# Kernel tuning notes

Hardware: AMD Instinct MI355X
Metric: run time of the kernel (lower is better)

Reference implementation:

```python
import jax, jax.numpy as jnp
import numpy as np

N = 6000          # nodes
E = 192000        # edges (avg degree 32)
D = 512           # input_dim
H = 512           # hidden_dim
O = 40            # output_dim (classes)
K = 4096          # codebook_size
LAMB_EDGE = 1.0
LAMB_NODE = 1.0
COMMIT_W = 0.25
EPS = 1e-12


def _graph_conv(x, W, b, src, dst):
    """DGL GraphConv with norm='both' + ReLU activation.
    out = relu( D_in^{-1/2} A D_out^{-1/2} x W + b )"""
    ones = jnp.ones((E,), x.dtype)
    deg_out = jnp.clip(jax.ops.segment_sum(ones, src, num_segments=N), 1.0)
    deg_in = jnp.clip(jax.ops.segment_sum(ones, dst, num_segments=N), 1.0)
    xs = x * jax.lax.rsqrt(deg_out)[:, None]          # scale by src out-degree
    agg = jax.ops.segment_sum(xs[src], dst, num_segments=N)  # gather-scatter
    agg = agg * jax.lax.rsqrt(deg_in)[:, None]        # scale by dst in-degree
    return jax.nn.relu(agg @ W + b)


def _l2norm(x):
    return x * jax.lax.rsqrt(jnp.sum(x * x, axis=-1, keepdims=True) + EPS)


def setup_inputs() -> dict:
    key = jax.random.key(0)
    ks = jax.random.split(key, 13)
    s = lambda d: 1.0 / np.sqrt(d)
    return {
        "feats": jax.random.normal(ks[0], (N, D), jnp.float32),
        "W1": jax.random.normal(ks[1], (D, D), jnp.float32) * s(D),
        "b1": jnp.zeros((D,), jnp.float32),
        "W2": jax.random.normal(ks[2], (D, H), jnp.float32) * s(D),
        "b2": jnp.zeros((H,), jnp.float32),
        "Wd1": jax.random.normal(ks[3], (D, D), jnp.float32) * s(D),
        "bd1": jnp.zeros((D,), jnp.float32),
        "Wd2": jax.random.normal(ks[4], (D, D), jnp.float32) * s(D),
        "bd2": jnp.zeros((D,), jnp.float32),
        "Wl": jax.random.normal(ks[5], (H, O), jnp.float32) * s(H),
        "bl": jnp.zeros((O,), jnp.float32),
        "codebook": jax.random.normal(ks[6], (K, D), jnp.float32),
        "src": jax.random.randint(ks[7], (E,), 0, N, jnp.int32),
        "dst": jax.random.randint(ks[8], (E,), 0, N, jnp.int32),
    }


def reference(feats, W1, b1, W2, b2, Wd1, bd1, Wd2, bd2, Wl, bl, codebook, src, dst):
    # dense adjacency (as the torch module materializes via to_dense())
    adj = jnp.zeros((N, N), feats.dtype).at[dst, src].add(1.0)

    # GraphConv layer 1 (dropout is identity in eval)
    h = _graph_conv(feats, W1, b1, src, dst)           # [N, D]

    # cosine-sim VectorQuantize
    hn = _l2norm(h)
    en = _l2norm(codebook)                             # [K, D]
    dist = hn @ en.T                                   # [N, K] cosine sims
    ind = jnp.argmax(dist, axis=-1)                    # [N]
    q = en[ind]                                        # quantize with normed codebook
    commit_loss = COMMIT_W * jnp.mean((jax.lax.stop_gradient(q) - h) ** 2)
    quantized = h + jax.lax.stop_gradient(q - h)       # straight-through

    quantized_edge = quantized @ Wd1 + bd1             # decoder_1
    quantized_node = quantized @ Wd2 + bd2             # decoder_2

    feature_rec_loss = LAMB_NODE * jnp.mean((h - quantized_node) ** 2)

    adj_q = quantized_edge @ quantized_edge.T          # [N, N]
    adj_q = (adj_q - adj_q.min()) / (adj_q.max() - adj_q.min())
    edge_rec_loss = LAMB_EDGE * jnp.sqrt(jnp.mean((adj - adj_q) ** 2))

    # GraphConv layer 2 + output linear
    h2 = _graph_conv(quantized_edge, W2, b2, src, dst) # [N, H]
    out = h2 @ Wl + bl                                 # [N, O]

    loss = feature_rec_loss + edge_rec_loss + commit_loss
    return out, loss, dist
```

## Files before the change

### kernel.cpp

```cpp
#include <hip/hip_runtime.h>

typedef unsigned int u32;
typedef unsigned long long u64;

#define NN_ 6000
#define EE_ 192000
#define DD_ 512
#define KK_ 4096
#define OO_ 40
#define HSZ (1 << 19)
#define HMASK (HSZ - 1)
#define MT_A 376
#define NB_N 47
#define WPACKE (32 * 16 * 512)

typedef __bf16 bf16x8 __attribute__((ext_vector_type(8)));
typedef float f32x4 __attribute__((ext_vector_type(4)));

__device__ __forceinline__ u32 okey(float f) {
    u32 u = __float_as_uint(f);
    return (u & 0x80000000u) ? ~u : (u | 0x80000000u);
}
__device__ __forceinline__ float dkey(u32 u) {
    u32 b = (u & 0x80000000u) ? (u ^ 0x80000000u) : ~u;
    return __uint_as_float(b);
}
__device__ __forceinline__ u64 packKey(float v, int col) {
    return ((u64)okey(v) << 32) | (u32)(~(u32)col);
}
__device__ __forceinline__ unsigned short f2bf_rne(float f) {
    u32 x = __float_as_uint(f);
    u32 r = x + 0x7fffu + ((x >> 16) & 1u);
    return (unsigned short)(r >> 16);
}
__device__ __forceinline__ void gld_lds16(void* l, const void* g) {
    __builtin_amdgcn_global_load_lds(
        (const __attribute__((address_space(1))) unsigned int*)g,
        (__attribute__((address_space(3))) unsigned int*)l, 16, 0, 0);
}
#define LGKM0 do { asm volatile("s_waitcnt lgkmcnt(0)" ::: "memory"); __builtin_amdgcn_sched_barrier(0); } while (0)

__global__ void k_deg(const int* __restrict__ src, const int* __restrict__ dst,
                      int* __restrict__ degout, int* __restrict__ degin) {
    int e = blockIdx.x * 256 + threadIdx.x;
    if (e >= EE_) return;
    atomicAdd(&degout[src[e]], 1);
    atomicAdd(&degin[dst[e]], 1);
}

__global__ void k_rsqrtdeg(const int* __restrict__ degout, const int* __restrict__ degin,
                           float* __restrict__ rout, float* __restrict__ rin) {
    int i = blockIdx.x * 256 + threadIdx.x;
    if (i >= NN_) return;
    int doV = degout[i]; if (doV < 1) doV = 1;
    int diV = degin[i];  if (diV < 1) diV = 1;
    rout[i] = rsqrtf((float)doV);
    rin[i]  = rsqrtf((float)diV);
}

__global__ void k_scan(const int* __restrict__ cnt, int* __restrict__ offs, int n) {
    __shared__ int buf[1024];
    __shared__ int carry;
    if (threadIdx.x == 0) { carry = 0; offs[0] = 0; }
    __syncthreads();
    for (int base = 0; base < n; base += 1024) {
        int i = base + threadIdx.x;
        int v = (i < n) ? cnt[i] : 0;
        buf[threadIdx.x] = v;
        __syncthreads();
        for (int off = 1; off < 1024; off <<= 1) {
            int t = (threadIdx.x >= off) ? buf[threadIdx.x - off] : 0;
            __syncthreads();
            buf[threadIdx.x] += t;
            __syncthreads();
        }
        if (i < n) offs[i + 1] = carry + buf[threadIdx.x];
        __syncthreads();
        if (threadIdx.x == 0) carry += buf[1023];
        __syncthreads();
    }
}

__global__ void k_fill(const int* __restrict__ src, const int* __restrict__ dst,
                       const int* __restrict__ offs, int* __restrict__ cursor,
                       int* __restrict__ esrc) {
    int e = blockIdx.x * 256 + threadIdx.x;
    if (e >= EE_) return;
    int d = dst[e];
    int pos = offs[d] + atomicAdd(&cursor[d], 1);
    esrc[pos] = src[e];
}

__device__ __forceinline__ void split8(const float* vals, uint4& hw, uint4& lw) {
    u32 h[4], l[4];
    #pragma unroll
    for (int j = 0; j < 4; ++j) {
        unsigned short h0 = f2bf_rne(vals[2*j]),   h1 = f2bf_rne(vals[2*j+1]);
        float hf0 = __uint_as_float((u32)h0 << 16), hf1 = __uint_as_float((u32)h1 << 16);
        unsigned short l0 = f2bf_rne(vals[2*j] - hf0), l1 = f2bf_rne(vals[2*j+1] - hf1);
        h[j] = (u32)h0 | ((u32)h1 << 16);
        l[j] = (u32)l0 | ((u32)l1 << 16);
    }
    hw = make_uint4(h[0], h[1], h[2], h[3]);
    lw = make_uint4(l[0], l[1], l[2], l[3]);
}

template<int UNW>
__global__ __launch_bounds__(256) void k_aggs(
    const float* __restrict__ X, const int* __restrict__ esrc,
    const int* __restrict__ offs, const float* __restrict__ rout,
    const float* __restrict__ rin,
    unsigned short* __restrict__ dh, unsigned short* __restrict__ dl,
    float* __restrict__ gacc) {
    __shared__ float packbuf[4][128];
    __shared__ float mred[4];
    int b = blockIdx.x;
    int xcd = b & 7;
    int slice = xcd >> 1;
    int w = threadIdx.x >> 6, lane = threadIdx.x & 63;
    int wid = ((((b >> 3) << 1) | (xcd & 1)) << 2) + w;
    const float* Xc = X + slice * 128 + lane * 2;
    float mrAcc = 0.f;
    for (int node = wid; node < NN_; node += 1024) {
        int beg = offs[node], end = offs[node + 1];
        float a0 = 0.f, a1 = 0.f, u0 = 0.f, u1 = 0.f;
        for (int e = beg; e < end; ) {
            int cnt = end - e; if (cnt > 64) cnt = 64;
            int sreg = 0; float wreg = 0.f;
            if (lane < cnt) { sreg = esrc[e + lane]; wreg = rout[sreg]; }
            int j = 0;
            for (; j + 4 <= cnt; j += 4) {
                int s0 = __shfl(sreg, j),     s1 = __shfl(sreg, j + 1);
                int s2 = __shfl(sreg, j + 2), s3 = __shfl(sreg, j + 3);
                float w0 = __shfl(wreg, j),     w1 = __shfl(wreg, j + 1);
                float w2 = __shfl(wreg, j + 2), w3 = __shfl(wreg, j + 3);
                float2 v0 = *(const float2*)(Xc + (size_t)s0 * DD_);
                float2 v1 = *(const float2*)(Xc + (size_t)s1 * DD_);
                float2 v2 = *(const float2*)(Xc + (size_t)s2 * DD_);
                float2 v3 = *(const float2*)(Xc + (size_t)s3 * DD_);
                a0 = fmaf(w0, v0.x, a0); a1 = fmaf(w0, v0.y, a1);
                a0 = fmaf(w1, v1.x, a0); a1 = fmaf(w1, v1.y, a1);
                a0 = fmaf(w2, v2.x, a0); a1 = fmaf(w2, v2.y, a1);
                a0 = fmaf(w3, v3.x, a0); a1 = fmaf(w3, v3.y, a1);
                if (UNW) {
                    u0 += (v0.x + v1.x) + (v2.x + v3.x);
                    u1 += (v0.y + v1.y) + (v2.y + v3.y);
                }
            }
            for (; j < cnt; ++j) {
                int sj = __shfl(sreg, j); float wj = __shfl(wreg, j);
                float2 v = *(const float2*)(Xc + (size_t)sj * DD_);
                a0 = fmaf(wj, v.x, a0); a1 = fmaf(wj, v.y, a1);
                if (UNW) { u0 += v.x; u1 += v.y; }
            }
            e += cnt;
        }
        float ri = rin[node];
        packbuf[w][lane * 2] = a0 * ri;
        packbuf[w][lane * 2 + 1] = a1 * ri;
        LGKM0;
        if (lane < 16) {
            uint4 hw, lw;
            split8(&packbuf[w][(lane >> 2) * 32 + (lane & 3) * 8], hw, lw);
            int kb = slice * 4 + (lane >> 2);
            int lo = (lane & 3) * 16 + (node & 15);
            size_t base = (((size_t)(node >> 4) * 16 + kb) * 64 + lo) * 8;
            *(uint4*)(dh + base) = hw;
            *(uint4*)(dl + base) = lw;
        }
        if (UNW) {
            float2 q = *(const float2*)(Xc + (size_t)node * DD_);
            mrAcc = fmaf(q.x, u0, mrAcc);
            mrAcc = fmaf(q.y, u1, mrAcc);
        }
    }
    if (UNW) {
        for (int off = 32; off; off >>= 1) mrAcc += __shfl_xor(mrAcc, off);
        if (lane == 0) mred[w] = mrAcc;
        __syncthreads();
        if (threadIdx.x == 0)
            atomicAdd(&gacc[5], mred[0] + mred[1] + mred[2] + mred[3]);
    }
}

__global__ __launch_bounds__(256) void k_cbscale(const float* __restrict__ cb,
                                                 float* __restrict__ scale, int nrows) {
    int w = threadIdx.x >> 6, lane = threadIdx.x & 63;
    for (int row = blockIdx.x * 4 + w; row < nrows; row += gridDim.x * 4) {
        const float4* p = (const float4*)(cb + (size_t)row * DD_);
        float4 x = p[lane], y = p[lane + 64];
        float s = x.x * x.x + x.y * x.y + x.z * x.z + x.w * x.w
                + y.x * y.x + y.y * y.y + y.z * y.z + y.w * y.w;
        for (int off = 32; off; off >>= 1) s += __shfl_xor(s, off);
        if (lane == 0) scale[row] = 1.0f / sqrtf(s + 1e-12f);
    }
}

__global__ __launch_bounds__(256) void k_pack(
    const float* __restrict__ src, const float* __restrict__ rowscale,
    const int* __restrict__ gidx, int nrows,
    unsigned short* __restrict__ dh, unsigned short* __restrict__ dl) {
    int u = threadIdx.x >> 6, lane = threadIdx.x & 63;
    int nmt = (nrows + 15) >> 4;
    for (int unit = blockIdx.x; unit < nmt * 4; unit += gridDim.x) {
        int mt = unit >> 2, kb = (unit & 3) * 4 + u;
        int gr = mt * 16 + (lane & 15);
        int k = kb * 32 + (lane >> 4) * 8;
        float vals[8] = {0.f,0.f,0.f,0.f,0.f,0.f,0.f,0.f};
        if (gr < nrows) {
            int row = gidx ? gidx[gr] : gr;
            float sc = rowscale ? rowscale[row] : 1.0f;
            const float4* p = (const float4*)(src + (size_t)row * DD_ + k);
            float4 a = p[0], bv = p[1];
            vals[0]=a.x*sc; vals[1]=a.y*sc; vals[2]=a.z*sc; vals[3]=a.w*sc;
            vals[4]=bv.x*sc; vals[5]=bv.y*sc; vals[6]=bv.z*sc; vals[7]=bv.w*sc;
        }
        uint4 hw, lw;
        split8(vals, hw, lw);
        size_t base = (((size_t)mt * 16 + kb) * 64 + lane) * 8;
        *(uint4*)(dh + base) = hw;
        *(uint4*)(dl + base) = lw;
    }
}

__global__ __launch_bounds__(256) void k_wpack(
    const float* __restrict__ W,
    unsigned short* __restrict__ dh, unsigned short* __restrict__ dl) {
    int u = threadIdx.x >> 6, lane = threadIdx.x & 63;
    int mt = blockIdx.x, kb = blockIdx.y * 4 + u;
    int n = mt * 16 + (lane & 15);
    int k = kb * 32 + (lane >> 4) * 8;
    float vals[8];
    #pragma unroll
    for (int j = 0; j < 8; ++j) vals[j] = W[(size_t)(k + j) * DD_ + n];
    uint4 hw, lw;
    split8(vals, hw, lw);
    size_t base = (((size_t)mt * 16 + kb) * 64 + lane) * 8;
    *(uint4*)(dh + base) = hw;
    *(uint4*)(dl + base) = lw;
}

template<int MODE, int THREE>
__global__ __launch_bounds__(256) void gemm_mfma(
    const unsigned short* __restrict__ Ah, const unsigned short* __restrict__ Al,
    const unsigned short* __restrict__ Bh, const unsigned short* __restrict__ Bl,
    float* __restrict__ Cout, const float* __restrict__ bias,
    const float* __restrict__ Ref, int relu, int Mrows,
    float* __restrict__ gacc, u32* __restrict__ minKey, u32* __restrict__ maxKey,
    const float* __restrict__ bias2) {
    int bx, by;
    if (MODE == 1) {
        int t = blockIdx.x;
        int bi = (int)((sqrtf(8.f * (float)t + 1.f) - 1.f) * 0.5f);
        while ((bi + 1) * (bi + 2) / 2 <= t) ++bi;
        while (bi * (bi + 1) / 2 > t) --bi;
        bx = bi; by = t - bi * (bi + 1) / 2;
    } else { bx = blockIdx.x; by = blockIdx.y; }
    int side = (MODE == 4) ? (bx >> 2) : 0;
    int bxe  = (MODE == 4) ? (bx & 3) : bx;
    __shared__ char lds[32768];
    __shared__ float wred0[4], wred1[4], wred2[4], wred3[4];
    int tid = threadIdx.x;
    int wave = tid >> 6, lane = tid & 63;
    int gmtA = by * 8, gmtB = bxe * 8;
    const unsigned short* garr; int gmt0;
    if (wave == 0)      { garr = Ah; gmt0 = gmtA; }
    else if (wave == 1) { garr = Al; gmt0 = gmtA; }
    else if (wave == 2) { garr = Bh + (size_t)side * 2 * WPACKE; gmt0 = gmtB; }
    else                { garr = Bl + (size_t)side * 2 * WPACKE; gmt0 = gmtB; }
    char* ldst = lds + wave * 8192;
    f32x4 acc[4][4];
    #pragma unroll
    for (int i = 0; i < 4; ++i)
        #pragma unroll
        for (int j = 0; j < 4; ++j) acc[i][j] = (f32x4){0.f, 0.f, 0.f, 0.f};
    float commitAcc = 0.f;
    int wm = wave >> 1, wn = wave & 1;
    for (int kb = 0; kb < 16; ++kb) {
        if (THREE || wave != 1) {
            #pragma unroll
            for (int t = 0; t < 8; ++t) {
                const char* g = (const char*)garr + (((size_t)(gmt0 + t) * 16 + kb) * 1024) + lane * 16;
                gld_lds16(ldst + t * 1024 + lane * 16, g);
            }
        }
        __syncthreads();
        if (MODE == 4 && bx == 4) {
            int rg = tid >> 1, half = tid & 1;
            int m = by * 128 + rg;
            if (m < Mrows) {
                int tt = rg >> 4, r = rg & 15;
                const float* hp = Ref + (size_t)m * DD_ + kb * 32 + half * 16;
                float4 h0 = ((const float4*)hp)[0], h1 = ((const float4*)hp)[1];
                float4 h2 = ((const float4*)hp)[2], h3 = ((const float4*)hp)[3];
                float hv[16] = {h0.x,h0.y,h0.z,h0.w, h1.x,h1.y,h1.z,h1.w,
                                h2.x,h2.y,h2.z,h2.w, h3.x,h3.y,h3.z,h3.w};
                #pragma unroll
                for (int j2 = 0; j2 < 16; ++j2) {
                    int sub = half * 2 + (j2 >> 3), j = j2 & 7;
                    int off = tt * 1024 + (sub * 16 + r) * 16 + j * 2;
                    u32 hb = *(const unsigned short*)(lds + off);
                    u32 lb = *(const unsigned short*)(lds + 8192 + off);
                    float q = __uint_as_float(hb << 16) + __uint_as_float(lb << 16);
                    float d = q - hv[j2];
                    commitAcc = fmaf(d, d, commitAcc);
                }
            }
        }
        bf16x8 a_h[4], a_l[4], b_h[4], b_l[4];
        #pragma unroll
        for (int i = 0; i < 4; ++i) {
            int at = wm * 4 + i, bt = wn * 4 + i;
            a_h[i] = *(const bf16x8*)(lds + 0     + at * 1024 + lane * 16);
            if (THREE) a_l[i] = *(const bf16x8*)(lds + 8192 + at * 1024 + lane * 16);
            b_h[i] = *(const bf16x8*)(lds + 16384 + bt * 1024 + lane * 16);
            b_l[i] = *(const bf16x8*)(lds + 24576 + bt * 1024 + lane * 16);
        }
        #pragma unroll
        for (int i = 0; i < 4; ++i)
            #pragma unroll
            for (int j = 0; j < 4; ++j) {
                acc[i][j] = __builtin_amdgcn_mfma_f32_16x16x32_bf16(a_h[i], b_h[j], acc[i][j], 0, 0, 0);
                acc[i][j] = __builtin_amdgcn_mfma_f32_16x16x32_bf16(a_h[i], b_l[j], acc[i][j], 0, 0, 0);
                if (THREE)
                    acc[i][j] = __builtin_amdgcn_mfma_f32_16x16x32_bf16(a_l[i], b_h[j], acc[i][j], 0, 0, 0);
            }
        __syncthreads();
    }
    int m_base = by * 128 + wm * 64;
    int n_base = bxe * 128 + wn * 64;
    int rq = lane >> 4, cc = lane & 15;
    if (MODE == 0) {
        #pragma unroll
        for (int i = 0; i < 4; ++i) {
            int m = m_base + i * 16 + rq * 4;
            #pragma unroll
            for (int j = 0; j < 4; ++j) {
                int n = n_base + j * 16 + cc;
                #pragma unroll
                for (int r = 0; r < 4; ++r) {
                    if (m + r < NN_) Cout[(size_t)(m + r) * KK_ + n] = acc[i][j][r];
                }
            }
        }
    } else if (MODE == 2 || (MODE == 4 && side == 0)) {
        #pragma unroll
        for (int i = 0; i < 4; ++i) {
            int m = m_base + i * 16 + rq * 4;
            #pragma unroll
            for (int j = 0; j < 4; ++j) {
                int n = n_base + j * 16 + cc;
                float bv = bias[n];
                #pragma unroll
                for (int r = 0; r < 4; ++r) {
                    if (m + r < Mrows) {
                        float v = acc[i][j][r] + bv;
                        if (relu) v = fmaxf(v, 0.f);
                        Cout[(size_t)(m + r) * DD_ + n] = v;
                    }
                }
            }
        }
    } else if (MODE == 3 || (MODE == 4 && side == 1)) {
        const float* bs = (MODE == 4) ? bias2 : bias;
        float s = 0.f;
        #pragma unroll
        for (int i = 0; i < 4; ++i) {
            int m = m_base + i * 16 + rq * 4;
            #pragma unroll
            for (int j = 0; j < 4; ++j) {
                int n = n_base + j * 16 + cc;
                float bv = bs[n];
                #pragma unroll
                for (int r = 0; r < 4; ++r) {
                    if (m + r < Mrows) {
                        float d = Ref[(size_t)(m + r) * DD_ + n] - (acc[i][j][r] + bv);
                        s = fmaf(d, d, s);
                    }
                }
            }
        }
        for (int off = 32; off; off >>= 1) s += __shfl_xor(s, off);
        if (lane == 0) wred0[wave] = s;
        if (MODE == 4 && bx == 4) {
            float c = commitAcc;
            for (int off = 32; off; off >>= 1) c += __shfl_xor(c, off);
            if (lane == 0) wred1[wave] = c;
        }
        __syncthreads();
        if (tid == 0) {
            atomicAdd(&gacc[3], wred0[0] + wred0[1] + wred0[2] + wred0[3]);
            if (MODE == 4 && bx == 4)
                atomicAdd(&gacc[2], wred1[0] + wred1[1] + wred1[2] + wred1[3]);
        }
    } else {
        float tsum = 0.f, tsq = 0.f, tmin = 3.4e38f, tmax = -3.4e38f;
        #pragma unroll
        for (int i = 0; i < 4; ++i) {
            #pragma unroll
            for (int j = 0; j < 4; ++j) {
                #pragma unroll
                for (int r = 0; r < 4; ++r) {
                    int m = m_base + i * 16 + rq * 4 + r;
                    int n = n_base + j * 16 + cc;
                    if (m < NN_ && n < NN_ && n >= m) {
                        float v = acc[i][j][r];
                        float w = (n > m) ? 2.f : 1.f;
                        tsum += w * v;
                        tsq  += w * v * v;
                        tmin = fminf(tmin, v);
                        tmax = fmaxf(tmax, v);
                    }
                }
            }
        }
        for (int off = 32; off; off >>= 1) {
            tsum += __shfl_xor(tsum, off);
            tsq  += __shfl_xor(tsq, off);
            tmin = fminf(tmin, __shfl_xor(tmin, off));
            tmax = fmaxf(tmax, __shfl_xor(tmax, off));
        }
        if (lane == 0) { wred0[wave] = tsum; wred1[wave] = tsq; wred2[wave] = tmin; wred3[wave] = tmax; }
        __syncthreads();
        if (tid == 0) {
            atomicAdd(&gacc[0], wred0[0] + wred0[1] + wred0[2] + wred0[3]);
            atomicAdd(&gacc[1], wred1[0] + wred1[1] + wred1[2] + wred1[3]);
            atomicMin(minKey, okey(fminf(fminf(wred2[0], wred2[1]), fminf(wred2[2], wred2[3]))));
            atomicMax(maxKey, okey(fmaxf(fmaxf(wred3[0], wred3[1]), fmaxf(wred3[2], wred3[3]))));
        }
    }
}

__global__ __launch_bounds__(256) void k_rescore(
    const float* __restrict__ dist, const float* __restrict__ h,
    const float* __restrict__ rnorm, const float* __restrict__ cb,
    const float* __restrict__ scale, int* __restrict__ ind) {
    int w = threadIdx.x >> 6, lane = threadIdx.x & 63;
    for (int row = blockIdx.x * 4 + w; row < NN_; row += gridDim.x * 4) {
        const float4* dr4 = (const float4*)(dist + (size_t)row * KK_);
        float4 vbuf[16];
        float lmax = -3.4e38f;
        #pragma unroll
        for (int it = 0; it < 16; ++it) {
            float4 v = dr4[lane + it * 64];
            vbuf[it] = v;
            lmax = fmaxf(lmax, fmaxf(fmaxf(v.x, v.y), fmaxf(v.z, v.w)));
        }
        for (int off = 32; off; off >>= 1) lmax = fmaxf(lmax, __shfl_xor(lmax, off));
        float thr = lmax - 1e-3f;
        float hr = rnorm[row];
        const float* hp = h + (size_t)row * DD_;
        u64 best = 0;
        #pragma unroll 1
        for (int it = 0; it < 16; ++it) {
            float4 v = vbuf[it];
            u32 m4 = (v.x >= thr ? 1u : 0u) | (v.y >= thr ? 2u : 0u)
                   | (v.z >= thr ? 4u : 0u) | (v.w >= thr ? 8u : 0u);
            u64 bal = __ballot(m4 != 0);
            while (bal) {
                int l = __ffsll((unsigned long long)bal) - 1;
                bal &= bal - 1;
                u32 mm = __shfl(m4, l);
                while (mm) {
                    int j = __ffs(mm) - 1;
                    mm &= mm - 1;
                    int col = (l + it * 64) * 4 + j;
                    const float* cp = cb + (size_t)col * DD_;
                    float dot = 0.f;
                    #pragma unroll
                    for (int jj = 0; jj < 8; ++jj)
                        dot = fmaf(hp[lane + jj * 64], cp[lane + jj * 64], dot);
                    for (int off = 32; off; off >>= 1) dot += __shfl_xor(dot, off);
                    u64 key = packKey(dot * hr * scale[col], col);
                    if (key > best) best = key;
                }
            }
        }
        if (lane == 0) ind[row] = (int)(~(u32)(best & 0xFFFFFFFFull));
    }
}

__global__ __launch_bounds__(256) void gemm_nn(
    const float* __restrict__ A, const float* __restrict__ B,
    const float* __restrict__ bias, float* __restrict__ C,
    int M, int Ncols, int Kdim) {
    __shared__ float As[16][68];
    __shared__ float Bs[16][68];
    int tid = threadIdx.x;
    int tx = tid & 15, ty = tid >> 4;
    int m0 = blockIdx.y * 64, n0 = blockIdx.x * 64;
    float cv[4][4] = {};
    int ar = tid >> 2;
    int ak = (tid & 3) << 2;
    int am = m0 + ar;
    const float* Arow = (am < M) ? (A + (size_t)am * Kdim) : nullptr;
    int bk = tid >> 4;
    int bn = (tid & 15) << 2;
    for (int k0 = 0; k0 < Kdim; k0 += 16) {
        float4 av = make_float4(0.f, 0.f, 0.f, 0.f);
        if (Arow) av = *(const float4*)(Arow + k0 + ak);
        As[ak + 0][ar] = av.x; As[ak + 1][ar] = av.y;
        As[ak + 2][ar] = av.z; As[ak + 3][ar] = av.w;
        float4 bv = make_float4(0.f, 0.f, 0.f, 0.f);
        if (n0 + bn < Ncols)
            bv = *(const float4*)(B + (size_t)(k0 + bk) * Ncols + n0 + bn);
        Bs[bk][bn + 0] = bv.x; Bs[bk][bn + 1] = bv.y;
        Bs[bk][bn + 2] = bv.z; Bs[bk][bn + 3] = bv.w;
        __syncthreads();
        #pragma unroll
        for (int kk = 0; kk < 16; ++kk) {
            float4 a4 = *(const float4*)&As[kk][ty << 2];
            float4 b4 = *(const float4*)&Bs[kk][tx << 2];
            float ax[4] = {a4.x, a4.y, a4.z, a4.w};
            float bx[4] = {b4.x, b4.y, b4.z, b4.w};
            #pragma unroll
            for (int i = 0; i < 4; ++i)
                #pragma unroll
                for (int j = 0; j < 4; ++j)
                    cv[i][j] = fmaf(ax[i], bx[j], cv[i][j]);
        }
        __syncthreads();
    }
    #pragma unroll
    for (int i = 0; i < 4; ++i) {
        int m = m0 + (ty << 2) + i;
        if (m >= M) continue;
        #pragma unroll
        for (int j = 0; j < 4; ++j) {
            int n = n0 + (tx << 2) + j;
            if (n >= Ncols) continue;
            C[(size_t)m * Ncols + n] = cv[i][j] + bias[n];
        }
    }
}

__global__ void k_hash(const int* __restrict__ src, const int* __restrict__ dst,
                       int* __restrict__ hkey, int* __restrict__ hcnt) {
    int e = blockIdx.x * 256 + threadIdx.x;
    if (e >= EE_) return;
    int key = dst[e] * NN_ + src[e];
    u32 h = ((u32)key * 2654435761u) & HMASK;
    while (true) {
        int old = atomicCAS(&hkey[h], -1, key);
        if (old == -1 || old == key) { atomicAdd(&hcnt[h], 1); break; }
        h = (h + 1) & HMASK;
    }
}

__global__ __launch_bounds__(256) void k_m2scan(const int* __restrict__ hcnt, float* __restrict__ gacc) {
    float s = 0.f;
    for (int i = blockIdx.x * 256 + threadIdx.x; i < HSZ; i += gridDim.x * 256) {
        float c = (float)hcnt[i];
        s = fmaf(c, c, s);
    }
    for (int off = 32; off; off >>= 1) s += __shfl_xor(s, off);
    __shared__ float w1[4];
    int lane = threadIdx.x & 63, wv = threadIdx.x >> 6;
    if (lane == 0) w1[wv] = s;
    __syncthreads();
    if (threadIdx.x == 0) atomicAdd(&gacc[4], w1[0] + w1[1] + w1[2] + w1[3]);
}

__global__ void k_final(const float* __restrict__ gacc, const u32* __restrict__ minKey,
                        const u32* __restrict__ maxKey, float* __restrict__ lossOut) {
    if (threadIdx.x != 0 || blockIdx.x != 0) return;
    double Rsum = gacc[0], Rsq = gacc[1], commitS = gacc[2], recS = gacc[3];
    double m2 = gacc[4], mr = gacc[5], ms = (double)EE_;
    double mn = (double)dkey(*minKey);
    double mx = (double)dkey(*maxKey);
    double den = mx - mn;
    double NN2 = (double)NN_ * (double)NN_;
    double sum_aq2 = (Rsq - 2.0 * mn * Rsum + NN2 * mn * mn) / (den * den);
    double sum_maq = (mr - mn * ms) / den;
    double total = sum_aq2 + m2 - 2.0 * sum_maq;
    double edge = sqrt(total / NN2);
    double commit = 0.25 * commitS / ((double)NN_ * (double)DD_);
    double rec = recS / ((double)NN_ * (double)DD_);
    *lossOut = (float)(rec + edge + commit);
}

extern "C" void kernel_launch(void* const* d_in, const int* in_sizes, int n_in,
                              void* d_out, int out_size, void* d_ws, size_t ws_size,
                              hipStream_t stream) {
    const float* feats = (const float*)d_in[0];
    const float* W1 = (const float*)d_in[1];
    const float* b1 = (const float*)d_in[2];
    const float* W2 = (const float*)d_in[3];
    const float* b2v = (const float*)d_in[4];
    const float* Wd1 = (const float*)d_in[5];
    const float* bd1 = (const float*)d_in[6];
    const float* Wd2 = (const float*)d_in[7];
    const float* bd2 = (const float*)d_in[8];
    const float* Wl = (const float*)d_in[9];
    const float* bl = (const float*)d_in[10];
    const float* cb = (const float*)d_in[11];
    const int* src = (const int*)d_in[12];
    const int* dst = (const int*)d_in[13];

    float* outF = (float*)d_out;
    float* lossOut = outF + (size_t)NN_ * OO_;
    float* distOut = lossOut + 1;

    char* w = (char*)d_ws;
    size_t off = 0;
    auto alloc = [&](size_t bytes) -> void* {
        void* p = w + off;
        off = (off + bytes + 255) & ~(size_t)255;
        return p;
    };
    float* gacc = (float*)alloc(64);
    u32* maxKey = (u32*)alloc(4);
    int* degin = (int*)alloc((size_t)NN_ * 4);
    int* degout = (int*)alloc((size_t)NN_ * 4);
    int* cursor = (int*)alloc((size_t)NN_ * 4);
    int* hcnt = (int*)alloc((size_t)HSZ * 4);
    size_t z0end = off;
    int* hkey = (int*)alloc((size_t)HSZ * 4);
    u32* minKey = (u32*)alloc(4);
    size_t z1end = off;
    int* offs = (int*)alloc((size_t)(NN_ + 1) * 4);
    int* esrc = (int*)alloc((size_t)EE_ * 4);
    float* rin = (float*)alloc((size_t)NN_ * 4);
    float* rout = (float*)alloc((size_t)NN_ * 4);
    int* ind = (int*)alloc((size_t)NN_ * 4);
    float* scale = (float*)alloc((size_t)KK_ * 4);
    float* rnorm = (float*)alloc((size_t)NN_ * 4);
    float* h = (float*)alloc((size_t)NN_ * DD_ * 4);
    float* QE = (float*)alloc((size_t)NN_ * DD_ * 4);
    const size_t NPACK = (size_t)MT_A * 16 * DD_;
    unsigned short* P1 = (unsigned short*)alloc(NPACK * 2 * 2);
    unsigned short* P2 = (unsigned short*)alloc(NPACK * 2 * 2);
    unsigned short* enp = (unsigned short*)alloc((size_t)KK_ * DD_ * 2 * 2);
    const size_t WPACK = (size_t)32 * 16 * DD_;
    unsigned short* W1p = (unsigned short*)alloc(WPACK * 2 * 2);
    unsigned short* Wd1p = (unsigned short*)alloc(WPACK * 2 * 2);
    unsigned short* Wd2p = (unsigned short*)alloc(WPACK * 2 * 2);
    unsigned short* W2p = (unsigned short*)alloc(WPACK * 2 * 2);

    unsigned short* aggp_h = P1,  *aggp_l = P1 + NPACK;
    unsigned short* qcp_h  = P1,  *qcp_l  = P1 + NPACK;
    unsigned short* ag2p_h = P1,  *ag2p_l = P1 + NPACK;
    unsigned short* hnp_h  = P2,  *hnp_l  = P2 + NPACK;
    unsigned short* QEp_h  = P2,  *QEp_l  = P2 + NPACK;
    unsigned short* enp_h  = enp, *enp_l  = enp + (size_t)KK_ * DD_;

    hipMemsetAsync(w, 0, z0end, stream);
    hipMemsetAsync(w + z0end, 0xFF, z1end - z0end, stream);

    const int TB = 256;
    k_deg<<<(EE_ + TB - 1) / TB, TB, 0, stream>>>(src, dst, degout, degin);
    k_rsqrtdeg<<<(NN_ + TB - 1) / TB, TB, 0, stream>>>(degout, degin, rout, rin);
    k_scan<<<1, 1024, 0, stream>>>(degin, offs, NN_);
    k_fill<<<(EE_ + TB - 1) / TB, TB, 0, stream>>>(src, dst, offs, cursor, esrc);
    k_wpack<<<dim3(32, 4), TB, 0, stream>>>(W1, W1p, W1p + WPACK);
    k_wpack<<<dim3(32, 4), TB, 0, stream>>>(Wd1, Wd1p, Wd1p + WPACK);
    k_wpack<<<dim3(32, 4), TB, 0, stream>>>(Wd2, Wd2p, Wd2p + WPACK);
    k_wpack<<<dim3(32, 4), TB, 0, stream>>>(W2, W2p, W2p + WPACK);
    k_aggs<0><<<1024, TB, 0, stream>>>(feats, esrc, offs, rout, rin, aggp_h, aggp_l, nullptr);
    gemm_mfma<2,1><<<dim3(4, NB_N), TB, 0, stream>>>(aggp_h, aggp_l, W1p, W1p + WPACK,
                                                     h, b1, nullptr, 1, NN_, nullptr, nullptr, nullptr, nullptr);
    k_cbscale<<<256, TB, 0, stream>>>(h, rnorm, NN_);
    k_cbscale<<<256, TB, 0, stream>>>(cb, scale, KK_);
    k_pack<<<512, TB, 0, stream>>>(h, rnorm, nullptr, NN_, hnp_h, hnp_l);
    k_pack<<<512, TB, 0, stream>>>(cb, scale, nullptr, KK_, enp_h, enp_l);
    gemm_mfma<0,0><<<dim3(KK_ / 128, NB_N), TB, 0, stream>>>(hnp_h, hnp_l, enp_h, enp_l,
                                                             distOut, nullptr, nullptr, 0, NN_,
                                                             nullptr, nullptr, nullptr, nullptr);
    k_rescore<<<1024, TB, 0, stream>>>(distOut, h, rnorm, cb, scale, ind);
    k_pack<<<512, TB, 0, stream>>>(cb, scale, ind, NN_, qcp_h, qcp_l);
    gemm_mfma<4,1><<<dim3(8, NB_N), TB, 0, stream>>>(qcp_h, qcp_l, Wd1p, Wd1p + WPACK,
                                                     QE, bd1, h, 0, NN_, gacc, nullptr, nullptr, bd2);
    k_pack<<<512, TB, 0, stream>>>(QE, nullptr, nullptr, NN_, QEp_h, QEp_l);
    gemm_mfma<1,1><<<NB_N * (NB_N + 1) / 2, TB, 0, stream>>>(QEp_h, QEp_l, QEp_h, QEp_l,
                                                             nullptr, nullptr, nullptr, 0, NN_,
                                                             gacc, minKey, maxKey, nullptr);
    k_hash<<<(EE_ + TB - 1) / TB, TB, 0, stream>>>(src, dst, hkey, hcnt);
    k_m2scan<<<512, TB, 0, stream>>>(hcnt, gacc);
    k_aggs<1><<<1024, TB, 0, stream>>>(QE, esrc, offs, rout, rin, ag2p_h, ag2p_l, gacc);
    gemm_mfma<2,1><<<dim3(4, NB_N), TB, 0, stream>>>(ag2p_h, ag2p_l, W2p, W2p + WPACK,
                                                     h, b2v, nullptr, 1, NN_, nullptr, nullptr, nullptr, nullptr);
    gemm_nn<<<dim3(1, 94), TB, 0, stream>>>(h, Wl, bl, outF, NN_, OO_, DD_);
    k_final<<<1, 64, 0, stream>>>(gacc, minKey, maxKey, lossOut);
}
```

Before: 681.0 us.

## Add dedicated 256x128-tile Gram kernel, fuse row-norm into pack, serial-chunk scan

A new gemm_rpass kernel replaces the triangular 128x128 MODE 1 path for the QE·QEᵀ min/max/sum reduction. Each block computes a 256x128 tile with eight accumulator rows per wave, and blocks are remapped over the upper triangle to cut redundant A/B loads and block count. The separate row-norm and pack kernels are merged into one row-oriented k_rowpack that computes the L2 scale and writes the packed bf16 hi/lo layout in one pass. k_scan now does a single-pass scan with 6 elements per thread instead of looping over 1024-element chunks. Risks are higher register pressure from acc[8][4] in the new kernel and uncoalesced scattered writes from the row-oriented pack.

```diff
diff --git a/kernel.cpp b/kernel.cpp
--- a/kernel.cpp
+++ b/kernel.cpp
@@ -59,25 +59,27 @@
 }
 
 __global__ void k_scan(const int* __restrict__ cnt, int* __restrict__ offs, int n) {
-    __shared__ int buf[1024];
-    __shared__ int carry;
-    if (threadIdx.x == 0) { carry = 0; offs[0] = 0; }
+    __shared__ int part[1024];
+    int t = threadIdx.x;
+    int base = t * 6;
+    int v[6]; int s = 0;
+    #pragma unroll
+    for (int j = 0; j < 6; ++j) { int i = base + j; v[j] = (i < n) ? cnt[i] : 0; s += v[j]; }
+    part[t] = s;
     __syncthreads();
-    for (int base = 0; base < n; base += 1024) {
-        int i = base + threadIdx.x;
-        int v = (i < n) ? cnt[i] : 0;
-        buf[threadIdx.x] = v;
-        __syncthreads();
-        for (int off = 1; off < 1024; off <<= 1) {
-            int t = (threadIdx.x >= off) ? buf[threadIdx.x - off] : 0;
-            __syncthreads();
-            buf[threadIdx.x] += t;
-            __syncthreads();
-        }
-        if (i < n) offs[i + 1] = carry + buf[threadIdx.x];
-        __syncthreads();
-        if (threadIdx.x == 0) carry += buf[1023];
-        __syncthreads();
+    for (int off = 1; off < 1024; off <<= 1) {
+        int x = (t >= off) ? part[t - off] : 0;
+        __syncthreads();
+        part[t] += x;
+        __syncthreads();
+    }
+    int run = (t > 0) ? part[t - 1] : 0;
+    if (t == 0) offs[0] = 0;
+    #pragma unroll
+    for (int j = 0; j < 6; ++j) {
+        int i = base + j;
+        run += v[j];
+        if (i < n) offs[i + 1] = run;
     }
 }
 
@@ -183,41 +185,30 @@
     }
 }
 
-__global__ __launch_bounds__(256) void k_cbscale(const float* __restrict__ cb,
-                                                 float* __restrict__ scale, int nrows) {
+template<int NORM>
+__global__ __launch_bounds__(256) void k_rowpack(
+    const float* __restrict__ src, const int* __restrict__ gidx,
+    const float* __restrict__ scaleIn, float* __restrict__ scaleOut, int nrows,
+    unsigned short* __restrict__ dh, unsigned short* __restrict__ dl) {
     int w = threadIdx.x >> 6, lane = threadIdx.x & 63;
-    for (int row = blockIdx.x * 4 + w; row < nrows; row += gridDim.x * 4) {
-        const float4* p = (const float4*)(cb + (size_t)row * DD_);
-        float4 x = p[lane], y = p[lane + 64];
-        float s = x.x * x.x + x.y * x.y + x.z * x.z + x.w * x.w
-                + y.x * y.x + y.y * y.y + y.z * y.z + y.w * y.w;
-        for (int off = 32; off; off >>= 1) s += __shfl_xor(s, off);
-        if (lane == 0) scale[row] = 1.0f / sqrtf(s + 1e-12f);
-    }
-}
-
-__global__ __launch_bounds__(256) void k_pack(
-    const float* __restrict__ src, const float* __restrict__ rowscale,
-    const int* __restrict__ gidx, int nrows,
-    unsigned short* __restrict__ dh, unsigned short* __restrict__ dl) {
-    int u = threadIdx.x >> 6, lane = threadIdx.x & 63;
-    int nmt = (nrows + 15) >> 4;
-    for (int unit = blockIdx.x; unit < nmt * 4; unit += gridDim.x) {
-        int mt = unit >> 2, kb = (unit & 3) * 4 + u;
-        int gr = mt * 16 + (lane & 15);
-        int k = kb * 32 + (lane >> 4) * 8;
-        float vals[8] = {0.f,0.f,0.f,0.f,0.f,0.f,0.f,0.f};
-        if (gr < nrows) {
-            int row = gidx ? gidx[gr] : gr;
-            float sc = rowscale ? rowscale[row] : 1.0f;
-            const float4* p = (const float4*)(src + (size_t)row * DD_ + k);
-            float4 a = p[0], bv = p[1];
-            vals[0]=a.x*sc; vals[1]=a.y*sc; vals[2]=a.z*sc; vals[3]=a.w*sc;
-            vals[4]=bv.x*sc; vals[5]=bv.y*sc; vals[6]=bv.z*sc; vals[7]=bv.w*sc;
-        }
+    for (int r = blockIdx.x * 4 + w; r < nrows; r += gridDim.x * 4) {
+        int rs = gidx ? gidx[r] : r;
+        const float4* p = (const float4*)(src + (size_t)rs * DD_);
+        float4 x = p[lane * 2], y = p[lane * 2 + 1];
+        float sc;
+        if (NORM) {
+            float s = x.x * x.x + x.y * x.y + x.z * x.z + x.w * x.w
+                    + y.x * y.x + y.y * y.y + y.z * y.z + y.w * y.w;
+            for (int off = 32; off; off >>= 1) s += __shfl_xor(s, off);
+            sc = 1.0f / sqrtf(s + 1e-12f);
+            if (scaleOut && lane == 0) scaleOut[r] = sc;
+        } else {
+            sc = scaleIn ? scaleIn[rs] : 1.0f;
+        }
+        float vals[8] = {x.x*sc, x.y*sc, x.z*sc, x.w*sc, y.x*sc, y.y*sc, y.z*sc, y.w*sc};
         uint4 hw, lw;
         split8(vals, hw, lw);
-        size_t base = (((size_t)mt * 16 + kb) * 64 + lane) * 8;
+        size_t base = (((size_t)(r >> 4) * 16 + (lane >> 2)) * 64 + (lane & 3) * 16 + (r & 15)) * 8;
         *(uint4*)(dh + base) = hw;
         *(uint4*)(dl + base) = lw;
     }
@@ -246,20 +237,12 @@
     const unsigned short* __restrict__ Bh, const unsigned short* __restrict__ Bl,
     float* __restrict__ Cout, const float* __restrict__ bias,
     const float* __restrict__ Ref, int relu, int Mrows,
-    float* __restrict__ gacc, u32* __restrict__ minKey, u32* __restrict__ maxKey,
-    const float* __restrict__ bias2) {
-    int bx, by;
-    if (MODE == 1) {
-        int t = blockIdx.x;
-        int bi = (int)((sqrtf(8.f * (float)t + 1.f) - 1.f) * 0.5f);
-        while ((bi + 1) * (bi + 2) / 2 <= t) ++bi;
-        while (bi * (bi + 1) / 2 > t) --bi;
-        bx = bi; by = t - bi * (bi + 1) / 2;
-    } else { bx = blockIdx.x; by = blockIdx.y; }
+    float* __restrict__ gacc, const float* __restrict__ bias2) {
+    int bx = blockIdx.x, by = blockIdx.y;
     int side = (MODE == 4) ? (bx >> 2) : 0;
     int bxe  = (MODE == 4) ? (bx & 3) : bx;
     __shared__ char lds[32768];
-    __shared__ float wred0[4], wred1[4], wred2[4], wred3[4];
+    __shared__ float wred0[4], wred1[4];
     int tid = threadIdx.x;
     int wave = tid >> 6, lane = tid & 63;
     int gmtA = by * 8, gmtB = bxe * 8;
@@ -361,8 +344,8 @@
                 }
             }
         }
-    } else if (MODE == 3 || (MODE == 4 && side == 1)) {
-        const float* bs = (MODE == 4) ? bias2 : bias;
+    } else {
+        const float* bs = bias2;
         float s = 0.f;
         #pragma unroll
         for (int i = 0; i < 4; ++i) {
@@ -393,41 +376,105 @@
             if (MODE == 4 && bx == 4)
                 atomicAdd(&gacc[2], wred1[0] + wred1[1] + wred1[2] + wred1[3]);
         }
-    } else {
-        float tsum = 0.f, tsq = 0.f, tmin = 3.4e38f, tmax = -3.4e38f;
-        #pragma unroll
-        for (int i = 0; i < 4; ++i) {
-            #pragma unroll
-            for (int j = 0; j < 4; ++j) {
+    }
+}
+
+__global__ __launch_bounds__(256) void gemm_rpass(
+    const unsigned short* __restrict__ Qh, const unsigned short* __restrict__ Ql,
+    float* __restrict__ gacc, u32* __restrict__ minKey, u32* __restrict__ maxKey) {
+    int Lp = blockIdx.x;
+    int L = (Lp & 7) * 72 + (Lp >> 3);
+    int b = (int)(24.f - sqrtf(576.f - (float)L));
+    if (b < 0) b = 0; if (b > 23) b = 23;
+    while (b * (48 - b) > L) --b;
+    while ((b + 1) * (47 - b) <= L) ++b;
+    int byp = b;
+    int bx = 2 * byp + (L - byp * (48 - byp));
+    __shared__ char lds[49152];
+    __shared__ float wr0[4], wr1[4], wr2[4], wr3[4];
+    int tid = threadIdx.x, wave = tid >> 6, lane = tid & 63;
+    int rh = wave >> 1, wn = wave & 1;
+    int gmtA0 = byp * 16;
+    int gmtA1 = (2 * byp + 1 <= 46) ? (2 * byp + 1) * 8 : 46 * 8;
+    int gmtB  = bx * 8;
+    f32x4 acc[8][4];
+    #pragma unroll
+    for (int i = 0; i < 8; ++i)
+        #pragma unroll
+        for (int j = 0; j < 4; ++j) acc[i][j] = (f32x4){0.f, 0.f, 0.f, 0.f};
+    for (int kb = 0; kb < 16; ++kb) {
+        #pragma unroll
+        for (int k = 0; k < 12; ++k) {
+            int g = wave * 12 + k;
+            int arr = g >> 3, mt = g & 7;
+            int gmt = (arr < 2) ? (gmtA0 + mt) : (arr < 4) ? (gmtA1 + mt) : (gmtB + mt);
+            const unsigned short* sp = (arr & 1) ? Ql : Qh;
+            gld_lds16(lds + arr * 8192 + mt * 1024 + lane * 16,
+                      (const char*)sp + (((size_t)gmt * 16 + kb) * 1024) + lane * 16);
+        }
+        __syncthreads();
+        bf16x8 b_h[4], b_l[4];
+        #pragma unroll
+        for (int j = 0; j < 4; ++j) {
+            b_h[j] = *(const bf16x8*)(lds + 32768 + (wn * 4 + j) * 1024 + lane * 16);
+            b_l[j] = *(const bf16x8*)(lds + 40960 + (wn * 4 + j) * 1024 + lane * 16);
+        }
+        #pragma unroll
+        for (int ih = 0; ih < 2; ++ih) {
+            bf16x8 a_h[4], a_l[4];
+            #pragma unroll
+            for (int z = 0; z < 4; ++z) {
+                a_h[z] = *(const bf16x8*)(lds + rh * 16384 + (ih * 4 + z) * 1024 + lane * 16);
+                a_l[z] = *(const bf16x8*)(lds + rh * 16384 + 8192 + (ih * 4 + z) * 1024 + lane * 16);
+            }
+            #pragma unroll
+            for (int z = 0; z < 4; ++z)
                 #pragma unroll
-                for (int r = 0; r < 4; ++r) {
-                    int m = m_base + i * 16 + rq * 4 + r;
-                    int n = n_base + j * 16 + cc;
-                    if (m < NN_ && n < NN_ && n >= m) {
-                        float v = acc[i][j][r];
-                        float w = (n > m) ? 2.f : 1.f;
-                        tsum += w * v;
-                        tsq  += w * v * v;
-                        tmin = fminf(tmin, v);
-                        tmax = fmaxf(tmax, v);
-                    }
+                for (int j = 0; j < 4; ++j) {
+                    int i = ih * 4 + z;
+                    acc[i][j] = __builtin_amdgcn_mfma_f32_16x16x32_bf16(a_h[z], b_h[j], acc[i][j], 0, 0, 0);
+                    acc[i][j] = __builtin_amdgcn_mfma_f32_16x16x32_bf16(a_h[z], b_l[j], acc[i][j], 0, 0, 0);
+                    acc[i][j] = __builtin_amdgcn_mfma_f32_16x16x32_bf16(a_l[z], b_h[j], acc[i][j], 0, 0, 0);
                 }
-            }
-        }
-        for (int off = 32; off; off >>= 1) {
-            tsum += __shfl_xor(tsum, off);
-            tsq  += __shfl_xor(tsq, off);
-            tmin = fminf(tmin, __shfl_xor(tmin, off));
-            tmax = fmaxf(tmax, __shfl_xor(tmax, off));
-        }
-        if (lane == 0) { wred0[wave] = tsum; wred1[wave] = tsq; wred2[wave] = tmin; wred3[wave] = tmax; }
-        __syncthreads();
-        if (tid == 0) {
-            atomicAdd(&gacc[0], wred0[0] + wred0[1] + wred0[2] + wred0[3]);
-            atomicAdd(&gacc[1], wred1[0] + wred1[1] + wred1[2] + wred1[3]);
-            atomicMin(minKey, okey(fminf(fminf(wred2[0], wred2[1]), fminf(wred2[2], wred2[3]))));
-            atomicMax(maxKey, okey(fmaxf(fmaxf(wred3[0], wred3[1]), fmaxf(wred3[2], wred3[3]))));
-        }
+        }
+        __syncthreads();
+    }
+    int m_base = byp * 256 + rh * 128;
+    int n_base = bx * 128 + wn * 64;
+    int rq = lane >> 4, cc = lane & 15;
+    float tsum = 0.f, tsq = 0.f, tmin = 3.4e38f, tmax = -3.4e38f;
+    #pragma unroll
+    for (int i = 0; i < 8; ++i) {
+        #pragma unroll
+        for (int j = 0; j < 4; ++j) {
+            #pragma unroll
+            for (int r = 0; r < 4; ++r) {
+                int m = m_base + i * 16 + rq * 4 + r;
+                int n = n_base + j * 16 + cc;
+                if (m < NN_ && n < NN_ && n >= m) {
+                    float v = acc[i][j][r];
+                    float w = (n > m) ? 2.f : 1.f;
+                    tsum += w * v;
+                    tsq  += w * v * v;
+                    tmin = fminf(tmin, v);
+                    tmax = fmaxf(tmax, v);
+                }
+            }
+        }
+    }
+    for (int off = 32; off; off >>= 1) {
+        tsum += __shfl_xor(tsum, off);
+        tsq  += __shfl_xor(tsq, off);
+        tmin = fminf(tmin, __shfl_xor(tmin, off));
+        tmax = fmaxf(tmax, __shfl_xor(tmax, off));
+    }
+    if (lane == 0) { wr0[wave] = tsum; wr1[wave] = tsq; wr2[wave] = tmin; wr3[wave] = tmax; }
+    __syncthreads();
+    if (tid == 0) {
+        atomicAdd(&gacc[0], wr0[0] + wr0[1] + wr0[2] + wr0[3]);
+        atomicAdd(&gacc[1], wr1[0] + wr1[1] + wr1[2] + wr1[3]);
+        atomicMin(minKey, okey(fminf(fminf(wr2[0], wr2[1]), fminf(wr2[2], wr2[3]))));
+        atomicMax(maxKey, okey(fmaxf(fmaxf(wr3[0], wr3[1]), fmaxf(wr3[2], wr3[3]))));
     }
 }
 
@@ -658,27 +705,23 @@
     k_wpack<<<dim3(32, 4), TB, 0, stream>>>(W2, W2p, W2p + WPACK);
     k_aggs<0><<<1024, TB, 0, stream>>>(feats, esrc, offs, rout, rin, aggp_h, aggp_l, nullptr);
     gemm_mfma<2,1><<<dim3(4, NB_N), TB, 0, stream>>>(aggp_h, aggp_l, W1p, W1p + WPACK,
-                                                     h, b1, nullptr, 1, NN_, nullptr, nullptr, nullptr, nullptr);
-    k_cbscale<<<256, TB, 0, stream>>>(h, rnorm, NN_);
-    k_cbscale<<<256, TB, 0, stream>>>(cb, scale, KK_);
-    k_pack<<<512, TB, 0, stream>>>(h, rnorm, nullptr, NN_, hnp_h, hnp_l);
-    k_pack<<<512, TB, 0, stream>>>(cb, scale, nullptr, KK_, enp_h, enp_l);
+                                                     h, b1, nullptr, 1, NN_, nullptr, nullptr);
+    k_rowpack<1><<<1024, TB, 0, stream>>>(h, nullptr, nullptr, rnorm, NN_, hnp_h, hnp_l);
+    k_rowpack<1><<<1024, TB, 0, stream>>>(cb, nullptr, nullptr, scale, KK_, enp_h, enp_l);
     gemm_mfma<0,0><<<dim3(KK_ / 128, NB_N), TB, 0, stream>>>(hnp_h, hnp_l, enp_h, enp_l,
                                                              distOut, nullptr, nullptr, 0, NN_,
-                                                             nullptr, nullptr, nullptr, nullptr);
+                                                             nullptr, nullptr);
     k_rescore<<<1024, TB, 0, stream>>>(distOut, h, rnorm, cb, scale, ind);
-    k_pack<<<512, TB, 0, stream>>>(cb, scale, ind, NN_, qcp_h, qcp_l);
+    k_rowpack<0><<<1024, TB, 0, stream>>>(cb, ind, scale, nullptr, NN_, qcp_h, qcp_l);
     gemm_mfma<4,1><<<dim3(8, NB_N), TB, 0, stream>>>(qcp_h, qcp_l, Wd1p, Wd1p + WPACK,
-                                                     QE, bd1, h, 0, NN_, gacc, nullptr, nullptr, bd2);
-    k_pack<<<512, TB, 0, stream>>>(QE, nullptr, nullptr, NN_, QEp_h, QEp_l);
-    gemm_mfma<1,1><<<NB_N * (NB_N + 1) / 2, TB, 0, stream>>>(QEp_h, QEp_l, QEp_h, QEp_l,
-                                                             nullptr, nullptr, nullptr, 0, NN_,
-                                                             gacc, minKey, maxKey, nullptr);
+                                                     QE, bd1, h, 0, NN_, gacc, bd2);
+    k_rowpack<0><<<1024, TB, 0, stream>>>(QE, nullptr, nullptr, nullptr, NN_, QEp_h, QEp_l);
+    gemm_rpass<<<576, TB, 0, stream>>>(QEp_h, QEp_l, gacc, minKey, maxKey);
     k_hash<<<(EE_ + TB - 1) / TB, TB, 0, stream>>>(src, dst, hkey, hcnt);
     k_m2scan<<<512, TB, 0, stream>>>(hcnt, gacc);
     k_aggs<1><<<1024, TB, 0, stream>>>(QE, esrc, offs, rout, rin, ag2p_h, ag2p_l, gacc);
     gemm_mfma<2,1><<<dim3(4, NB_N), TB, 0, stream>>>(ag2p_h, ag2p_l, W2p, W2p + WPACK,
-                                                     h, b2v, nullptr, 1, NN_, nullptr, nullptr, nullptr, nullptr);
+                                                     h, b2v, nullptr, 1, NN_, nullptr, nullptr);
     gemm_nn<<<dim3(1, 94), TB, 0, stream>>>(h, Wl, bl, outF, NN_, OO_, DD_);
     k_final<<<1, 64, 0, stream>>>(gacc, minKey, maxKey, lossOut);
 }
```

Measured after the change: 688.3 us. Within noise of the previous version (+1.1%).
